# Optimization experiments

Hardware: AMD Instinct MI355X
Metric: run time of the kernel (lower is better)

## Reference

```python
import jax, jax.numpy as jnp
import numpy as np

BRANCH = 4
DEPTH = 5
D = 512
N_NODES = (BRANCH ** (DEPTH + 1) - 1) // (BRANCH - 1)  # 1365
BATCH = 16


def setup_inputs() -> dict:
    key = jax.random.key(0)
    k1, k2, k3 = jax.random.split(key, 3)
    inputs = jax.random.normal(k1, (BATCH, D), dtype=jnp.float32)
    # per-node Linear(512,512) weights, torch layout [out, in], scaled like kaiming-ish init
    W = jax.random.normal(k2, (N_NODES, D, D), dtype=jnp.float32) * (1.0 / np.sqrt(D))
    b = jax.random.normal(k3, (N_NODES, D), dtype=jnp.float32) * 0.01
    return {"inputs": inputs, "W": W, "b": b}


def reference(inputs, W, b):
    # BFS over a complete BRANCH-ary tree; node i>0 has parent (i-1)//BRANCH.
    # Root: Linear only (no relu, per source); children: relu(Linear(parent_act)).
    # All nodes at one BFS level are batched into a single grouped einsum.
    acts = []
    a = inputs @ W[0].T + b[0]          # [B, D] root, no relu
    acts.append(a[:, None, :])
    prev = acts[0]                       # [B, level_size, D]
    prev_start = 0
    start = 1
    for lvl in range(1, DEPTH + 1):
        sz = BRANCH ** lvl
        idx = np.arange(start, start + sz)
        parent_local = (idx - 1) // BRANCH - prev_start  # indices into prev level
        pa = prev[:, parent_local, :]                    # [B, sz, D]
        Wl = W[start:start + sz]                         # [sz, D(out), D(in)]
        bl = b[start:start + sz]                         # [sz, D]
        a = jax.nn.relu(jnp.einsum('bnd,nhd->bnh', pa, Wl) + bl)  # [B, sz, D]
        acts.append(a)
        prev = a
        prev_start = start
        start += sz
    out = jnp.concatenate(acts, axis=1)                  # [B, N_NODES, D]
    return out.reshape(out.shape[0], -1)                 # [B, N_NODES*D], like torch.cat(dim=1)
```

## Files before the change

### kernel.cpp

```cpp
#include <hip/hip_runtime.h>

#define D 512
#define NNODES 1365
#define OUT_STRIDE (NNODES * D)

typedef __attribute__((ext_vector_type(4))) float f32x4;
typedef __attribute__((ext_vector_type(8))) short bf16x8;

union U4 { uint4 q; unsigned u[4]; bf16x8 v; };

__device__ inline unsigned cvt_pk_bf16(float s0, float s1) {
    unsigned r;
    asm volatile("v_cvt_pk_bf16_f32 %0, %1, %2" : "=v"(r) : "v"(s0), "v"(s1));
    return r;
}

__device__ inline void gld_lds16(const void* g, void* l) {
    __builtin_amdgcn_global_load_lds(
        (const __attribute__((address_space(1))) unsigned*)g,
        (__attribute__((address_space(3))) unsigned*)l, 16, 0, 0);
}

template<int G, bool RELU>
__global__ __launch_bounds__(256, 2)
void node_kernel(const float* __restrict__ W,
                 const float* __restrict__ bias,
                 const float* __restrict__ src_base,
                 float* __restrict__ out,
                 int node_start, int bpn, int src_stride)
{
    __shared__ float Wt[4][2][16 * 128];

    const int tid  = threadIdx.x;
    const int w    = tid >> 6;
    const int lane = tid & 63;
    const int m4   = lane >> 4;
    const int c0   = lane & 15;

    const int node  = node_start + blockIdx.x / bpn;
    const int nbase = (blockIdx.x % bpn) * (64 * G);

    const float* Wn = W + (size_t)node * (D * D);

    const int rr  = lane >> 5;
    const int off = (lane & 31) * 16;
    auto issue_chunk = [&](int g, int q) {
        char* ldst = (char*)&Wt[w][(g * 4 + q) & 1][0];
        const char* gsrc = (const char*)Wn +
            (size_t)(nbase + (g * 4 + w) * 16) * 2048 + q * 512;
        #pragma unroll
        for (int i = 0; i < 8; ++i) {
            const int r = i * 2 + rr;
            gld_lds16(gsrc + (size_t)r * 2048 + (off ^ ((r & 7) << 4)),
                      ldst + i * 1024);
        }
    };

    float bv[G];
    #pragma unroll
    for (int g = 0; g < G; ++g) {
        bv[g] = bias[(size_t)node * D + nbase + (g * 4 + w) * 16 + c0];
        asm volatile("" :: "v"(bv[g]));
    }

    issue_chunk(0, 0);
    issue_chunk(0, 1);

    const float* arow = (RELU ? src_base + (size_t)((node - 1) >> 2) * D
                              : src_base) + (size_t)c0 * src_stride;
    bf16x8 aH[16], aL[16];
    #pragma unroll
    for (int j = 0; j < 16; ++j) {
        const float* p = arow + j * 32 + m4 * 8;
        float4 x0 = *(const float4*)p;
        float4 x1 = *(const float4*)(p + 4);
        float xs[8] = {x0.x,x0.y,x0.z,x0.w,x1.x,x1.y,x1.z,x1.w};
        U4 h, l;
        #pragma unroll
        for (int k = 0; k < 4; ++k) {
            unsigned hh = cvt_pk_bf16(xs[2*k], xs[2*k+1]);
            float f0 = __uint_as_float(hh << 16);
            float f1 = __uint_as_float(hh & 0xFFFF0000u);
            l.u[k] = cvt_pk_bf16(xs[2*k] - f0, xs[2*k+1] - f1);
            h.u[k] = hh;
        }
        aH[j] = h.v; aL[j] = l.v;
    }

    f32x4 acc = {0.f, 0.f, 0.f, 0.f};
    #pragma unroll
    for (int g = 0; g < G; ++g) {
        #pragma unroll
        for (int q = 0; q < 4; ++q) {
            if (q == 0) {
                if (g == 0) asm volatile("s_waitcnt vmcnt(8)"  ::: "memory");
                else        asm volatile("s_waitcnt vmcnt(12)" ::: "memory");
            } else if (q == 3 && g == G - 1) {
                asm volatile("s_waitcnt vmcnt(0)"  ::: "memory");
            } else {
                asm volatile("s_waitcnt vmcnt(8)"  ::: "memory");
            }

            const char* tb = (const char*)&Wt[w][(g * 4 + q) & 1][0];
            const int rsw = (c0 & 7) << 4;
            #pragma unroll
            for (int ks = 0; ks < 4; ++ks) {
                const int kb = ks * 128 + m4 * 32;
                float4 b0 = *(const float4*)(tb + c0 * 512 + (kb ^ rsw));
                float4 b1 = *(const float4*)(tb + c0 * 512 + ((kb + 16) ^ rsw));
                U4 bH, bL;
                float xs[8] = {b0.x,b0.y,b0.z,b0.w,b1.x,b1.y,b1.z,b1.w};
                #pragma unroll
                for (int k = 0; k < 4; ++k) {
                    unsigned hh = cvt_pk_bf16(xs[2*k], xs[2*k+1]);
                    float f0 = __uint_as_float(hh << 16);
                    float f1 = __uint_as_float(hh & 0xFFFF0000u);
                    bL.u[k] = cvt_pk_bf16(xs[2*k] - f0, xs[2*k+1] - f1);
                    bH.u[k] = hh;
                }
                const int j = q * 4 + ks;
                acc = __builtin_amdgcn_mfma_f32_16x16x32_bf16(aH[j], bH.v, acc, 0,0,0);
                acc = __builtin_amdgcn_mfma_f32_16x16x32_bf16(aL[j], bH.v, acc, 0,0,0);
                acc = __builtin_amdgcn_mfma_f32_16x16x32_bf16(aH[j], bL.v, acc, 0,0,0);
            }

            if (q == 0)      issue_chunk(g, 2);
            else if (q == 1) issue_chunk(g, 3);
            else if (g < G - 1) {
                if (q == 2) issue_chunk(g + 1, 0);
                else        issue_chunk(g + 1, 1);
            }

            if (q == 3) {
                const int wcol = node * D + nbase + (g * 4 + w) * 16 + c0;
                #pragma unroll
                for (int i = 0; i < 4; ++i) {
                    float v = acc[i] + bv[g];
                    if (RELU) v = fmaxf(v, 0.f);
                    out[(size_t)(m4 * 4 + i) * OUT_STRIDE + wcol] = v;
                }
                acc = (f32x4){0.f, 0.f, 0.f, 0.f};
            }
        }
    }
}

extern "C" void kernel_launch(void* const* d_in, const int* in_sizes, int n_in,
                              void* d_out, int out_size, void* d_ws, size_t ws_size,
                              hipStream_t stream) {
    const float* inputs = (const float*)d_in[0];
    const float* W      = (const float*)d_in[1];
    const float* bias   = (const float*)d_in[2];
    float* out          = (float*)d_out;

    node_kernel<1, false><<<   8, 256, 0, stream>>>(W, bias, inputs, out,   0, 8, D);
    node_kernel<1, true ><<<  32, 256, 0, stream>>>(W, bias, out,    out,   1, 8, OUT_STRIDE);
    node_kernel<1, true ><<< 128, 256, 0, stream>>>(W, bias, out,    out,   5, 8, OUT_STRIDE);
    node_kernel<1, true ><<< 512, 256, 0, stream>>>(W, bias, out,    out,  21, 8, OUT_STRIDE);
    node_kernel<4, true ><<< 512, 256, 0, stream>>>(W, bias, out,    out,  85, 2, OUT_STRIDE);
    node_kernel<8, true ><<<1024, 256, 0, stream>>>(W, bias, out,    out, 341, 1, OUT_STRIDE);
}
```

Baseline: 345.5 us.

## Split node work into 4-row chunks to spread tree levels over more blocks

Each wave now loads a 4-output-row by 512-K chunk of W (instead of a 16x128 slab) and computes a full-K dot for 4 output columns per chunk. This allows much finer splitting of each node across blocks, so the small early levels and the last level launch many more blocks to fill the GPU. The cost is that only 4 of 16 MFMA output columns are useful: MFMA work per byte grows and the A fragments are replicated. The LDS layout and prefetch schedule are reworked to fit.

```diff
diff --git a/kernel.cpp b/kernel.cpp
--- a/kernel.cpp
+++ b/kernel.cpp
@@ -21,7 +21,7 @@
         (__attribute__((address_space(3))) unsigned*)l, 16, 0, 0);
 }
 
-template<int G, bool RELU>
+template<int NC, bool RELU>
 __global__ __launch_bounds__(256, 2)
 void node_kernel(const float* __restrict__ W,
                  const float* __restrict__ bias,
@@ -29,7 +29,7 @@
                  float* __restrict__ out,
                  int node_start, int bpn, int src_stride)
 {
-    __shared__ float Wt[4][2][16 * 128];
+    __shared__ float Wt[4][2][2048];
 
     const int tid  = threadIdx.x;
     const int w    = tid >> 6;
@@ -38,33 +38,28 @@
     const int c0   = lane & 15;
 
     const int node  = node_start + blockIdx.x / bpn;
-    const int nbase = (blockIdx.x % bpn) * (64 * G);
-
+    const int nbase = (blockIdx.x % bpn) * (16 * NC);
     const float* Wn = W + (size_t)node * (D * D);
 
-    const int rr  = lane >> 5;
-    const int off = (lane & 31) * 16;
-    auto issue_chunk = [&](int g, int q) {
-        char* ldst = (char*)&Wt[w][(g * 4 + q) & 1][0];
+    const int drow = ((lane >> 2) & 1) + 2 * ((lane >> 3) & 1);
+    const int loff = drow * 2048 +
+        ((lane >> 5) * 8 + (lane & 3) * 2 + ((lane >> 4) & 1)) * 16;
+
+    auto issue_chunk = [&](int c) {
         const char* gsrc = (const char*)Wn +
-            (size_t)(nbase + (g * 4 + w) * 16) * 2048 + q * 512;
+            (size_t)(nbase + (c * 4 + w) * 4) * 2048 + loff;
+        char* ldst = (char*)&Wt[w][c & 1][0];
         #pragma unroll
-        for (int i = 0; i < 8; ++i) {
-            const int r = i * 2 + rr;
-            gld_lds16(gsrc + (size_t)r * 2048 + (off ^ ((r & 7) << 4)),
-                      ldst + i * 1024);
-        }
+        for (int i = 0; i < 8; ++i)
+            gld_lds16(gsrc + i * 256, ldst + i * 1024);
     };
 
-    float bv[G];
+    float bf[NC];
     #pragma unroll
-    for (int g = 0; g < G; ++g) {
-        bv[g] = bias[(size_t)node * D + nbase + (g * 4 + w) * 16 + c0];
-        asm volatile("" :: "v"(bv[g]));
+    for (int c = 0; c < NC; ++c) {
+        bf[c] = bias[(size_t)node * D + nbase + (c * 4 + w) * 4 + (c0 & 3)];
+        asm volatile("" :: "v"(bf[c]));
     }
-
-    issue_chunk(0, 0);
-    issue_chunk(0, 1);
 
     const float* arow = (RELU ? src_base + (size_t)((node - 1) >> 2) * D
                               : src_base) + (size_t)c0 * src_stride;
@@ -87,59 +82,49 @@
         aH[j] = h.v; aL[j] = l.v;
     }
 
-    f32x4 acc = {0.f, 0.f, 0.f, 0.f};
+    issue_chunk(0);
+    if (NC > 1) issue_chunk(1);
+
+    const int laneoff = ((c0 >> 1) & 1) * 128 + (c0 & 1) * 64 + m4 * 16;
+
     #pragma unroll
-    for (int g = 0; g < G; ++g) {
+    for (int c = 0; c < NC; ++c) {
+        if      (c == NC - 1) asm volatile("s_waitcnt vmcnt(0)"  ::: "memory");
+        else if (c == 0)      asm volatile("s_waitcnt vmcnt(8)"  ::: "memory");
+        else if (c == 1)      asm volatile("s_waitcnt vmcnt(12)" ::: "memory");
+        else                  asm volatile("s_waitcnt vmcnt(16)" ::: "memory");
+
+        const char* tb = (const char*)&Wt[w][c & 1][0];
+        f32x4 acc = {0.f, 0.f, 0.f, 0.f};
         #pragma unroll
-        for (int q = 0; q < 4; ++q) {
-            if (q == 0) {
-                if (g == 0) asm volatile("s_waitcnt vmcnt(8)"  ::: "memory");
-                else        asm volatile("s_waitcnt vmcnt(12)" ::: "memory");
-            } else if (q == 3 && g == G - 1) {
-                asm volatile("s_waitcnt vmcnt(0)"  ::: "memory");
-            } else {
-                asm volatile("s_waitcnt vmcnt(8)"  ::: "memory");
+        for (int ks = 0; ks < 16; ++ks) {
+            float4 b0 = *(const float4*)(tb + ks * 512 + laneoff);
+            float4 b1 = *(const float4*)(tb + ks * 512 + laneoff + 256);
+            U4 bH, bL;
+            float xs[8] = {b0.x,b0.y,b0.z,b0.w,b1.x,b1.y,b1.z,b1.w};
+            #pragma unroll
+            for (int k = 0; k < 4; ++k) {
+                unsigned hh = cvt_pk_bf16(xs[2*k], xs[2*k+1]);
+                float f0 = __uint_as_float(hh << 16);
+                float f1 = __uint_as_float(hh & 0xFFFF0000u);
+                bL.u[k] = cvt_pk_bf16(xs[2*k] - f0, xs[2*k+1] - f1);
+                bH.u[k] = hh;
             }
+            acc = __builtin_amdgcn_mfma_f32_16x16x32_bf16(aH[ks], bH.v, acc, 0,0,0);
+            acc = __builtin_amdgcn_mfma_f32_16x16x32_bf16(aL[ks], bH.v, acc, 0,0,0);
+            acc = __builtin_amdgcn_mfma_f32_16x16x32_bf16(aH[ks], bL.v, acc, 0,0,0);
+        }
 
-            const char* tb = (const char*)&Wt[w][(g * 4 + q) & 1][0];
-            const int rsw = (c0 & 7) << 4;
+        if (c + 2 < NC) issue_chunk(c + 2);
+
+        if (c0 < 4) {
+            const int wcol = node * D + nbase + (c * 4 + w) * 4 + c0;
+            const float bv = bf[c];
             #pragma unroll
-            for (int ks = 0; ks < 4; ++ks) {
-                const int kb = ks * 128 + m4 * 32;
-                float4 b0 = *(const float4*)(tb + c0 * 512 + (kb ^ rsw));
-                float4 b1 = *(const float4*)(tb + c0 * 512 + ((kb + 16) ^ rsw));
-                U4 bH, bL;
-                float xs[8] = {b0.x,b0.y,b0.z,b0.w,b1.x,b1.y,b1.z,b1.w};
-                #pragma unroll
-                for (int k = 0; k < 4; ++k) {
-                    unsigned hh = cvt_pk_bf16(xs[2*k], xs[2*k+1]);
-                    float f0 = __uint_as_float(hh << 16);
-                    float f1 = __uint_as_float(hh & 0xFFFF0000u);
-                    bL.u[k] = cvt_pk_bf16(xs[2*k] - f0, xs[2*k+1] - f1);
-                    bH.u[k] = hh;
-                }
-                const int j = q * 4 + ks;
-                acc = __builtin_amdgcn_mfma_f32_16x16x32_bf16(aH[j], bH.v, acc, 0,0,0);
-                acc = __builtin_amdgcn_mfma_f32_16x16x32_bf16(aL[j], bH.v, acc, 0,0,0);
-                acc = __builtin_amdgcn_mfma_f32_16x16x32_bf16(aH[j], bL.v, acc, 0,0,0);
-            }
-
-            if (q == 0)      issue_chunk(g, 2);
-            else if (q == 1) issue_chunk(g, 3);
-            else if (g < G - 1) {
-                if (q == 2) issue_chunk(g + 1, 0);
-                else        issue_chunk(g + 1, 1);
-            }
-
-            if (q == 3) {
-                const int wcol = node * D + nbase + (g * 4 + w) * 16 + c0;
-                #pragma unroll
-                for (int i = 0; i < 4; ++i) {
-                    float v = acc[i] + bv[g];
-                    if (RELU) v = fmaxf(v, 0.f);
-                    out[(size_t)(m4 * 4 + i) * OUT_STRIDE + wcol] = v;
-                }
-                acc = (f32x4){0.f, 0.f, 0.f, 0.f};
+            for (int i = 0; i < 4; ++i) {
+                float v = acc[i] + bv;
+                if (RELU) v = fmaxf(v, 0.f);
+                out[(size_t)(m4 * 4 + i) * OUT_STRIDE + wcol] = v;
             }
         }
     }
@@ -153,10 +138,10 @@
     const float* bias   = (const float*)d_in[2];
     float* out          = (float*)d_out;
 
-    node_kernel<1, false><<<   8, 256, 0, stream>>>(W, bias, inputs, out,   0, 8, D);
-    node_kernel<1, true ><<<  32, 256, 0, stream>>>(W, bias, out,    out,   1, 8, OUT_STRIDE);
-    node_kernel<1, true ><<< 128, 256, 0, stream>>>(W, bias, out,    out,   5, 8, OUT_STRIDE);
-    node_kernel<1, true ><<< 512, 256, 0, stream>>>(W, bias, out,    out,  21, 8, OUT_STRIDE);
-    node_kernel<4, true ><<< 512, 256, 0, stream>>>(W, bias, out,    out,  85, 2, OUT_STRIDE);
-    node_kernel<8, true ><<<1024, 256, 0, stream>>>(W, bias, out,    out, 341, 1, OUT_STRIDE);
+    node_kernel<1, false><<<  32, 256, 0, stream>>>(W, bias, inputs, out,   0, 32, D);
+    node_kernel<1, true ><<< 128, 256, 0, stream>>>(W, bias, out,    out,   1, 32, OUT_STRIDE);
+    node_kernel<2, true ><<< 256, 256, 0, stream>>>(W, bias, out,    out,   5, 16, OUT_STRIDE);
+    node_kernel<4, true ><<< 512, 256, 0, stream>>>(W, bias, out,    out,  21,  8, OUT_STRIDE);
+    node_kernel<8, true ><<<1024, 256, 0, stream>>>(W, bias, out,    out,  85,  4, OUT_STRIDE);
+    node_kernel<8, true ><<<4096, 256, 0, stream>>>(W, bias, out,    out, 341,  4, OUT_STRIDE);
 }
```

Measured after the change: 428.7 us. 24.1% more time.
